# Kernel tuning notes

Measured on AMD Instinct MI355X. Metric: run time of the kernel, lower is better.

Reference implementation:

```python
import jax, jax.numpy as jnp
import numpy as np

B, S, NODE, DEP, R, L, E = 32, 1024, 256, 64, 50, 16, 128


def setup_inputs() -> dict:
    key = jax.random.key(0)
    k1, k2, k3, k4, k5 = jax.random.split(key, 5)
    context = jax.random.normal(k1, (B, S, NODE), dtype=jnp.float32)
    # torch.rand -> uniform [0,1); one [dep, node+dep] matrix per dependency relation
    dep_W = jax.random.uniform(k2, (R, DEP, NODE + DEP), dtype=jnp.float32)
    heads = jax.random.randint(k3, (B, L, E), 0, S, dtype=jnp.int32)
    tails = jax.random.randint(k4, (B, L, E), 0, S, dtype=jnp.int32)
    rels = jax.random.randint(k5, (B, L, E), 0, R, dtype=jnp.int32)
    return {"context": context, "dep_W": dep_W, "heads": heads, "tails": tails, "rels": rels}


def reference(context, dep_W, heads, tails, rels):
    # context: [B,S,node]; dep_W: [R,dep,node+dep]; heads/tails/rels: [B,L,E]
    B_, S_, node = context.shape
    dep = dep_W.shape[1]
    E_ = heads.shape[2]
    batch_off = jnp.arange(B_, dtype=jnp.int32)[:, None] * S_  # [B,1]

    def layer_step(child, layer):
        h, t, r = layer  # each [B,E]
        # gather per-edge tail features (node feature ++ child state from deeper layers)
        ctx_t = jnp.take_along_axis(context, t[:, :, None], axis=1)  # [B,E,node]
        chd_t = jnp.take_along_axis(child, t[:, :, None], axis=1)    # [B,E,dep]
        feat = jnp.concatenate([ctx_t, chd_t], axis=-1)              # [B,E,node+dep]
        W_e = dep_W[r]                                               # [B,E,dep,node+dep]
        # sum(W * feat, dim=1) == relation-indexed matvec
        msg = jnp.einsum('bekd,bed->bek', W_e, feat)                 # [B,E,dep]
        # scatter-average messages onto head nodes (per batch -> flat index)
        idx = (batch_off + h).reshape(-1)                            # [B*E]
        seg = jax.ops.segment_sum(msg.reshape(-1, dep), idx, num_segments=B_ * S_)
        cnt = jax.ops.segment_sum(jnp.ones((B_ * E_,), msg.dtype), idx, num_segments=B_ * S_)
        avg = seg / jnp.maximum(cnt, 1.0)[:, None]
        child_flat = child.reshape(B_ * S_, dep)
        # heads touched this layer get the averaged message (assignment semantics)
        child_new = jnp.where((cnt > 0)[:, None], avg, child_flat).reshape(B_, S_, dep)
        return child_new, None

    child0 = jnp.zeros((B_, S_, dep), context.dtype)
    layers = (jnp.moveaxis(heads, 1, 0), jnp.moveaxis(tails, 1, 0), jnp.moveaxis(rels, 1, 0))
    child, _ = jax.lax.scan(layer_step, child0, layers)  # layer 0 = deepest layer
    return jnp.concatenate([context, child], axis=-1)    # [B,S,node+dep]
```

## Files before the change

kernel.cpp:

```cpp
#include <hip/hip_runtime.h>

constexpr int B_ = 32;
constexpr int S_ = 1024;
constexpr int NODE_ = 256;
constexpr int DEP_ = 64;
constexpr int R_ = 50;
constexpr int L_ = 16;
constexpr int E_ = 128;
constexpr int FEAT_ = NODE_ + DEP_;
constexpr int NEDGE_ = B_ * E_;
constexpr int BS_ = B_ * S_;
constexpr int CH_ = 16;
constexpr int NCH_ = 320;
constexpr int PREB_ = 512;

constexpr size_t N_CHILD  = (size_t)BS_ * DEP_;
constexpr size_t OFF_A0   = N_CHILD;
constexpr size_t OFF_WT   = N_CHILD * 4;
constexpr size_t N_WT     = (size_t)R_ * FEAT_ * DEP_;
constexpr size_t OFF_SORT = OFF_WT + N_WT;
constexpr size_t N_SORT   = (size_t)L_ * NEDGE_;
constexpr size_t OFF_CHUNK= OFF_SORT + N_SORT;
constexpr size_t N_CHUNK_I= (size_t)L_ * NCH_ * 4;
constexpr size_t OFF_HC   = OFF_CHUNK + N_CHUNK_I;
constexpr size_t N_HC     = (size_t)L_ * BS_;
constexpr size_t OFF_MT   = OFF_HC + N_HC;
constexpr size_t OFF_MH   = OFF_MT + N_SORT;
constexpr size_t OFF_MI   = OFF_MH + N_SORT;
constexpr size_t OFF_CD   = OFF_MI + N_SORT;
constexpr size_t N_CD     = (size_t)L_ * NEDGE_ * DEP_;

__global__ void k_pre(const float* __restrict__ W, const int* __restrict__ rels,
                      const int* __restrict__ heads,
                      float* __restrict__ WT2, int* __restrict__ sorted,
                      int4* __restrict__ chunks, int* __restrict__ hc,
                      float* __restrict__ zero_base) {
  int blk = blockIdx.x, tid = threadIdx.x;
  if (blk < L_) {
    int l = blk;
    __shared__ int hist[R_], startA[R_], rank[R_], cstart[R_];
    __shared__ int ntot;
    if (tid < R_) { hist[tid] = 0; rank[tid] = 0; }
    int* hcl = hc + (size_t)l * BS_;
    for (int i = tid; i < BS_; i += 256) hcl[i] = 0;
    __syncthreads();
    for (int ed = tid; ed < NEDGE_; ed += 256) {
      int b = ed >> 7, e = ed & (E_ - 1);
      atomicAdd(&hist[rels[(b * L_ + l) * E_ + e]], 1);
      atomicAdd(&hcl[b * S_ + heads[(b * L_ + l) * E_ + e]], 1);
    }
    __syncthreads();
    if (tid == 0) {
      int s = 0, cs = 0;
      for (int r = 0; r < R_; ++r) {
        startA[r] = s; s += hist[r];
        cstart[r] = cs; cs += (hist[r] + CH_ - 1) / CH_;
      }
      ntot = cs;
    }
    __syncthreads();
    for (int ed = tid; ed < NEDGE_; ed += 256) {
      int b = ed >> 7, e = ed & (E_ - 1);
      int r = rels[(b * L_ + l) * E_ + e];
      int pos = startA[r] + atomicAdd(&rank[r], 1);
      sorted[l * NEDGE_ + pos] = ed;
    }
    if (tid < R_) {
      int n = hist[tid], st = startA[tid], cs = cstart[tid];
      for (int m = 0; m * CH_ < n; ++m) {
        int c = n - m * CH_; if (c > CH_) c = CH_;
        chunks[l * NCH_ + cs + m] = make_int4(tid, st + m * CH_, c, 0);
      }
    }
    __syncthreads();
    for (int i = ntot + tid; i < NCH_; i += 256)
      chunks[l * NCH_ + i] = make_int4(0, 0, 0, 0);
  } else {
    int gtid = (blk - L_) * 256 + tid;
    const int NT = PREB_ * 256;
    for (int gid = gtid; gid < (int)N_WT; gid += NT) {
      int r = gid / 20480;
      int rem = gid - r * 20480;
      int i4 = rem >> 8;
      int k = (rem >> 2) & 63;
      int c = rem & 3;
      WT2[gid] = W[((size_t)r * DEP_ + k) * FEAT_ + 4 * i4 + c];
    }
    float4* z4 = (float4*)zero_base;
    int nz4 = (int)((N_CHILD * 2) / 4);
    for (int i = gtid; i < nz4; i += NT) z4[i] = make_float4(0.f, 0.f, 0.f, 0.f);
  }
}

__device__ __forceinline__ float dot64(const float4* __restrict__ f4,
                                       const float4* __restrict__ w) {
  float a0 = 0.f, a1 = 0.f, a2 = 0.f, a3 = 0.f;
#pragma unroll
  for (int i = 0; i < 16; ++i) {
    float4 f = f4[i];
    a0 = fmaf(w[i].x, f.x, a0);
    a1 = fmaf(w[i].y, f.y, a1);
    a2 = fmaf(w[i].z, f.z, a2);
    a3 = fmaf(w[i].w, f.w, a3);
  }
  return (a0 + a1) + (a2 + a3);
}

__global__ void __launch_bounds__(256) k_ctx(
    const float* __restrict__ context, const float* __restrict__ WT2,
    const int* __restrict__ heads, const int* __restrict__ tails,
    const int* __restrict__ sorted, const int4* __restrict__ chunks,
    const int* __restrict__ hc, float* __restrict__ ctxdot,
    int* __restrict__ m_trow, int* __restrict__ m_hrow,
    float* __restrict__ m_invc) {
  int cid = blockIdx.x;
  int l = cid / NCH_;
  int4 ck = chunks[cid];
  int r = ck.x, start = ck.y, ccnt = ck.z;
  if (ccnt == 0) return;
  int tid = threadIdx.x, s = tid >> 6, k = tid & 63;

  __shared__ float feat[CH_][NODE_];
  __shared__ float part[4][CH_][DEP_];
  __shared__ int trows[CH_];
  __shared__ float invs[CH_];

  if (tid < ccnt) {
    int pos = l * NEDGE_ + start + tid;
    int ed = sorted[pos];
    int b = ed >> 7, e = ed & (E_ - 1);
    int t = tails[(b * L_ + l) * E_ + e];
    int h = heads[(b * L_ + l) * E_ + e];
    int trow = b * S_ + t, hrow = b * S_ + h;
    int tch = (l > 0) && (hc[(size_t)(l - 1) * BS_ + trow] > 0);
    float invc = 1.0f / (float)hc[(size_t)l * BS_ + hrow];
    m_trow[pos] = trow | (tch ? (int)0x80000000 : 0);
    m_hrow[pos] = hrow;
    m_invc[pos] = invc;
    trows[tid] = trow;
    invs[tid] = invc;
  }
  __syncthreads();

  int tr[CH_];
#pragma unroll
  for (int j = 0; j < CH_; ++j) tr[j] = trows[(j < ccnt) ? j : (ccnt - 1)];

  const float4* Wp = (const float4*)WT2 + ((size_t)r * 80 + s * 16) * 64 + k;
  float4 w[16];
#pragma unroll
  for (int i = 0; i < 16; ++i) w[i] = Wp[(size_t)i * 64];

#pragma unroll
  for (int j = 0; j < CH_; ++j)
    feat[j][tid] = context[(size_t)tr[j] * NODE_ + tid];
  __syncthreads();

  for (int j = 0; j < ccnt; ++j)
    part[s][j][k] = dot64((const float4*)&feat[j][s * 64], w);
  __syncthreads();

  for (int idx = tid; idx < ccnt * DEP_; idx += 256) {
    int j = idx >> 6, k2 = idx & 63;
    ctxdot[(size_t)(l * NEDGE_ + start + j) * DEP_ + k2] =
        (part[0][j][k2] + part[1][j][k2] + part[2][j][k2] + part[3][j][k2]) *
        invs[j];
  }
}

__global__ void __launch_bounds__(256) k_layer(
    const float* __restrict__ WT2, float* __restrict__ child,
    const int4* __restrict__ chunks, const int* __restrict__ m_trow,
    const int* __restrict__ m_hrow, const float* __restrict__ m_invc,
    const float* __restrict__ ctxdot, int l,
    const float* __restrict__ Aprev, float* __restrict__ Acur,
    float* __restrict__ Anext) {
  int tid = threadIdx.x;
  int4 ck = chunks[l * NCH_ + blockIdx.x];
  int r = ck.x, start = ck.y, ccnt = ck.z;
  __shared__ float feat[CH_][DEP_];

  if (ccnt > 0) {
    int wv = tid >> 6, k = tid & 63;

    const float4* Wp = (const float4*)WT2 + ((size_t)r * 80 + 64) * 64 + k;
    float4 w[16];
#pragma unroll
    for (int i = 0; i < 16; ++i) w[i] = Wp[(size_t)i * 64];

    int jj[4], valid[4], tch[4], trow[4], hrow[4];
    float invc[4];
#pragma unroll
    for (int u = 0; u < 4; ++u) {
      int j = wv + 4 * u;
      valid[u] = (j < ccnt);
      jj[u] = valid[u] ? j : (ccnt - 1);
      int pos = l * NEDGE_ + start + jj[u];
      int tr = m_trow[pos];
      tch[u] = (tr < 0);
      trow[u] = tr & 0x7fffffff;
      hrow[u] = m_hrow[pos];
      invc[u] = m_invc[pos];
    }

    float v[4];
#pragma unroll
    for (int u = 0; u < 4; ++u) {
      const float* p = tch[u] ? Aprev : child;
      v[u] = p[(size_t)trow[u] * DEP_ + k];
    }
#pragma unroll
    for (int u = 0; u < 4; ++u) feat[jj[u]][k] = v[u];
    __syncthreads();

#pragma unroll
    for (int u = 0; u < 4; ++u) {
      float d = dot64((const float4*)&feat[jj[u]][0], w);
      int pos = l * NEDGE_ + start + jj[u];
      float contrib = d * invc[u] + ctxdot[(size_t)pos * DEP_ + k];
      if (valid[u]) atomicAdd(&Acur[(size_t)hrow[u] * DEP_ + k], contrib);
    }
  }

  int gtid = blockIdx.x * 256 + tid;
  const int NT = NCH_ * 256;
  if (l > 0) {
    const float4* Ap4 = (const float4*)Aprev;
    float4* ch4 = (float4*)child;
    const int* mh = m_hrow + (size_t)(l - 1) * NEDGE_;
    for (int idx = gtid; idx < NEDGE_ * 16; idx += NT) {
      int pos = idx >> 4, c4 = idx & 15;
      int hrow = mh[pos];
      ch4[(size_t)hrow * 16 + c4] = Ap4[(size_t)hrow * 16 + c4];
    }
  }
  if (l + 1 < L_) {
    float4* An4 = (float4*)Anext;
    const int* mh = m_hrow + (size_t)(l + 1) * NEDGE_;
    float4 z = make_float4(0.f, 0.f, 0.f, 0.f);
    for (int idx = gtid; idx < NEDGE_ * 16; idx += NT) {
      int pos = idx >> 4, c4 = idx & 15;
      An4[(size_t)mh[pos] * 16 + c4] = z;
    }
  }
}

__global__ void k_out(const float4* __restrict__ ctx4,
                      const float4* __restrict__ chd4,
                      const float4* __restrict__ A04,
                      const int* __restrict__ hc15,
                      float4* __restrict__ out4) {
  constexpr int TOT4 = B_ * S_ * (FEAT_ / 4);
  int i = blockIdx.x * blockDim.x + threadIdx.x;
  if (i >= TOT4) return;
  int row = i / 80;
  int c4 = i - row * 80;
  float4 v;
  if (c4 < 64) {
    v = ctx4[(size_t)row * 64 + c4];
  } else {
    int k4 = c4 - 64;
    v = (hc15[row] > 0) ? A04[(size_t)row * 16 + k4]
                        : chd4[(size_t)row * 16 + k4];
  }
  out4[i] = v;
}

extern "C" void kernel_launch(void* const* d_in, const int* in_sizes, int n_in,
                              void* d_out, int out_size, void* d_ws, size_t ws_size,
                              hipStream_t stream) {
  const float* context = (const float*)d_in[0];
  const float* dep_W   = (const float*)d_in[1];
  const int*   heads   = (const int*)d_in[2];
  const int*   tails   = (const int*)d_in[3];
  const int*   rels    = (const int*)d_in[4];
  float* out = (float*)d_out;

  float* ws = (float*)d_ws;
  float* child  = ws;
  float* A[3] = { ws + OFF_A0, ws + OFF_A0 + N_CHILD, ws + OFF_A0 + 2 * N_CHILD };
  float* WT2    = ws + OFF_WT;
  int*   sorted = (int*)(ws + OFF_SORT);
  int4*  chunks = (int4*)(ws + OFF_CHUNK);
  int*   hc     = (int*)(ws + OFF_HC);
  int*   m_trow = (int*)(ws + OFF_MT);
  int*   m_hrow = (int*)(ws + OFF_MH);
  float* m_invc = ws + OFF_MI;
  float* ctxdot = ws + OFF_CD;

  k_pre<<<L_ + PREB_, 256, 0, stream>>>(dep_W, rels, heads, WT2, sorted,
                                        chunks, hc, child);

  k_ctx<<<L_ * NCH_, 256, 0, stream>>>(context, WT2, heads, tails, sorted,
                                       chunks, hc, ctxdot, m_trow, m_hrow,
                                       m_invc);

  for (int l = 0; l < L_; ++l) {
    float* Acur  = A[l % 3];
    float* Aprev = A[(l + 2) % 3];
    float* Anext = A[(l + 1) % 3];
    k_layer<<<NCH_, 256, 0, stream>>>(WT2, child, chunks, m_trow, m_hrow,
                                      m_invc, ctxdot, l, Aprev, Acur, Anext);
  }

  constexpr int TOT4 = B_ * S_ * (FEAT_ / 4);
  k_out<<<(TOT4 + 255) / 256, 256, 0, stream>>>(
      (const float4*)context, (const float4*)child, (const float4*)A[0],
      hc + (size_t)(L_ - 1) * BS_, (float4*)out);
}
```

Measured before the change: 313.0 us.

## Fuse per-layer launches and output copy into one cooperative persistent kernel

Replaces the sixteen per-layer kernel launches and the separate output kernel with one cooperative kernel. It loops over layers and uses a grid-wide sync between them, then writes the output at the end. k_ctx and the layer dot products now read context/child rows straight from global memory with wave-uniform indices instead of staging them through shared memory. This removes launch gaps and shared-memory round trips. The cost is that only 256 blocks handle the 320 chunks, and the final copy runs on a smaller grid.

Result: slower. 938.0 us (+199.7%).

```diff
diff --git a/kernel.cpp b/kernel.cpp
--- a/kernel.cpp
+++ b/kernel.cpp
@@ -1,4 +1,7 @@
 #include <hip/hip_runtime.h>
+#include <hip/hip_cooperative_groups.h>
+
+namespace cg = cooperative_groups;
 
 constexpr int B_ = 32;
 constexpr int S_ = 1024;
@@ -13,6 +16,7 @@
 constexpr int CH_ = 16;
 constexpr int NCH_ = 320;
 constexpr int PREB_ = 512;
+constexpr int GRID_ = 256;
 
 constexpr size_t N_CHILD  = (size_t)BS_ * DEP_;
 constexpr size_t OFF_A0   = N_CHILD;
@@ -92,20 +96,6 @@
   }
 }
 
-__device__ __forceinline__ float dot64(const float4* __restrict__ f4,
-                                       const float4* __restrict__ w) {
-  float a0 = 0.f, a1 = 0.f, a2 = 0.f, a3 = 0.f;
-#pragma unroll
-  for (int i = 0; i < 16; ++i) {
-    float4 f = f4[i];
-    a0 = fmaf(w[i].x, f.x, a0);
-    a1 = fmaf(w[i].y, f.y, a1);
-    a2 = fmaf(w[i].z, f.z, a2);
-    a3 = fmaf(w[i].w, f.w, a3);
-  }
-  return (a0 + a1) + (a2 + a3);
-}
-
 __global__ void __launch_bounds__(256) k_ctx(
     const float* __restrict__ context, const float* __restrict__ WT2,
     const int* __restrict__ heads, const int* __restrict__ tails,
@@ -120,9 +110,7 @@
   if (ccnt == 0) return;
   int tid = threadIdx.x, s = tid >> 6, k = tid & 63;
 
-  __shared__ float feat[CH_][NODE_];
   __shared__ float part[4][CH_][DEP_];
-  __shared__ int trows[CH_];
   __shared__ float invs[CH_];
 
   if (tid < ccnt) {
@@ -137,27 +125,34 @@
     m_trow[pos] = trow | (tch ? (int)0x80000000 : 0);
     m_hrow[pos] = hrow;
     m_invc[pos] = invc;
-    trows[tid] = trow;
     invs[tid] = invc;
   }
-  __syncthreads();
-
-  int tr[CH_];
-#pragma unroll
-  for (int j = 0; j < CH_; ++j) tr[j] = trows[(j < ccnt) ? j : (ccnt - 1)];
 
   const float4* Wp = (const float4*)WT2 + ((size_t)r * 80 + s * 16) * 64 + k;
   float4 w[16];
 #pragma unroll
   for (int i = 0; i < 16; ++i) w[i] = Wp[(size_t)i * 64];
 
-#pragma unroll
-  for (int j = 0; j < CH_; ++j)
-    feat[j][tid] = context[(size_t)tr[j] * NODE_ + tid];
-  __syncthreads();
-
-  for (int j = 0; j < ccnt; ++j)
-    part[s][j][k] = dot64((const float4*)&feat[j][s * 64], w);
+#pragma unroll 4
+  for (int j = 0; j < CH_; ++j) {
+    int jc = (j < ccnt) ? j : (ccnt - 1);
+    int pos = l * NEDGE_ + start + jc;
+    int ed = __builtin_amdgcn_readfirstlane(sorted[pos]);
+    int b = ed >> 7, e = ed & (E_ - 1);
+    int t = __builtin_amdgcn_readfirstlane(tails[(b * L_ + l) * E_ + e]);
+    const float4* fp =
+        (const float4*)(context + ((size_t)(b * S_ + t)) * NODE_ + s * 64);
+    float a0 = 0.f, a1 = 0.f, a2 = 0.f, a3 = 0.f;
+#pragma unroll
+    for (int i = 0; i < 16; ++i) {
+      float4 f = fp[i];
+      a0 = fmaf(w[i].x, f.x, a0);
+      a1 = fmaf(w[i].y, f.y, a1);
+      a2 = fmaf(w[i].z, f.z, a2);
+      a3 = fmaf(w[i].w, f.w, a3);
+    }
+    part[s][jc][k] = (a0 + a1) + (a2 + a3);
+  }
   __syncthreads();
 
   for (int idx = tid; idx < ccnt * DEP_; idx += 256) {
@@ -168,102 +163,98 @@
   }
 }
 
-__global__ void __launch_bounds__(256) k_layer(
+__global__ void __launch_bounds__(256) k_chain(
     const float* __restrict__ WT2, float* __restrict__ child,
     const int4* __restrict__ chunks, const int* __restrict__ m_trow,
     const int* __restrict__ m_hrow, const float* __restrict__ m_invc,
-    const float* __restrict__ ctxdot, int l,
-    const float* __restrict__ Aprev, float* __restrict__ Acur,
-    float* __restrict__ Anext) {
-  int tid = threadIdx.x;
-  int4 ck = chunks[l * NCH_ + blockIdx.x];
-  int r = ck.x, start = ck.y, ccnt = ck.z;
-  __shared__ float feat[CH_][DEP_];
-
-  if (ccnt > 0) {
-    int wv = tid >> 6, k = tid & 63;
-
-    const float4* Wp = (const float4*)WT2 + ((size_t)r * 80 + 64) * 64 + k;
-    float4 w[16];
-#pragma unroll
-    for (int i = 0; i < 16; ++i) w[i] = Wp[(size_t)i * 64];
-
-    int jj[4], valid[4], tch[4], trow[4], hrow[4];
-    float invc[4];
-#pragma unroll
-    for (int u = 0; u < 4; ++u) {
-      int j = wv + 4 * u;
-      valid[u] = (j < ccnt);
-      jj[u] = valid[u] ? j : (ccnt - 1);
-      int pos = l * NEDGE_ + start + jj[u];
-      int tr = m_trow[pos];
-      tch[u] = (tr < 0);
-      trow[u] = tr & 0x7fffffff;
-      hrow[u] = m_hrow[pos];
-      invc[u] = m_invc[pos];
-    }
-
-    float v[4];
-#pragma unroll
-    for (int u = 0; u < 4; ++u) {
-      const float* p = tch[u] ? Aprev : child;
-      v[u] = p[(size_t)trow[u] * DEP_ + k];
-    }
-#pragma unroll
-    for (int u = 0; u < 4; ++u) feat[jj[u]][k] = v[u];
-    __syncthreads();
-
-#pragma unroll
-    for (int u = 0; u < 4; ++u) {
-      float d = dot64((const float4*)&feat[jj[u]][0], w);
-      int pos = l * NEDGE_ + start + jj[u];
-      float contrib = d * invc[u] + ctxdot[(size_t)pos * DEP_ + k];
-      if (valid[u]) atomicAdd(&Acur[(size_t)hrow[u] * DEP_ + k], contrib);
-    }
-  }
-
-  int gtid = blockIdx.x * 256 + tid;
-  const int NT = NCH_ * 256;
-  if (l > 0) {
-    const float4* Ap4 = (const float4*)Aprev;
-    float4* ch4 = (float4*)child;
-    const int* mh = m_hrow + (size_t)(l - 1) * NEDGE_;
-    for (int idx = gtid; idx < NEDGE_ * 16; idx += NT) {
-      int pos = idx >> 4, c4 = idx & 15;
-      int hrow = mh[pos];
-      ch4[(size_t)hrow * 16 + c4] = Ap4[(size_t)hrow * 16 + c4];
-    }
-  }
-  if (l + 1 < L_) {
-    float4* An4 = (float4*)Anext;
-    const int* mh = m_hrow + (size_t)(l + 1) * NEDGE_;
-    float4 z = make_float4(0.f, 0.f, 0.f, 0.f);
-    for (int idx = gtid; idx < NEDGE_ * 16; idx += NT) {
-      int pos = idx >> 4, c4 = idx & 15;
-      An4[(size_t)mh[pos] * 16 + c4] = z;
-    }
-  }
-}
-
-__global__ void k_out(const float4* __restrict__ ctx4,
-                      const float4* __restrict__ chd4,
-                      const float4* __restrict__ A04,
-                      const int* __restrict__ hc15,
-                      float4* __restrict__ out4) {
+    const float* __restrict__ ctxdot, float* __restrict__ Abase,
+    const int* __restrict__ hc15, const float4* __restrict__ ctx4,
+    float4* __restrict__ out4) {
+  cg::grid_group grid = cg::this_grid();
+  int tid = threadIdx.x, wv = tid >> 6, k = tid & 63;
+
+  for (int l = 0; l < L_; ++l) {
+    float* Acur        = Abase + (size_t)(l % 3) * N_CHILD;
+    const float* Aprev = Abase + (size_t)((l + 2) % 3) * N_CHILD;
+    float* Anext       = Abase + (size_t)((l + 1) % 3) * N_CHILD;
+
+    for (int cid = blockIdx.x; cid < NCH_; cid += gridDim.x) {
+      int4 ck = chunks[l * NCH_ + cid];
+      int r = ck.x, start = ck.y, ccnt = ck.z;
+      if (ccnt == 0) continue;
+
+      const float4* Wp = (const float4*)WT2 + ((size_t)r * 80 + 64) * 64 + k;
+      float4 w[16];
+#pragma unroll
+      for (int i = 0; i < 16; ++i) w[i] = Wp[(size_t)i * 64];
+
+#pragma unroll
+      for (int u = 0; u < 4; ++u) {
+        int j = wv + 4 * u;
+        bool valid = (j < ccnt);
+        int jc = valid ? j : 0;
+        int pos = l * NEDGE_ + start + jc;
+        int tr = __builtin_amdgcn_readfirstlane(m_trow[pos]);
+        int hrow = __builtin_amdgcn_readfirstlane(m_hrow[pos]);
+        float invc = m_invc[pos];
+        int trow = tr & 0x7fffffff;
+        const float* base = (tr < 0) ? Aprev : child;
+        const float4* fp = (const float4*)(base + (size_t)trow * DEP_);
+        float a0 = 0.f, a1 = 0.f, a2 = 0.f, a3 = 0.f;
+#pragma unroll
+        for (int i = 0; i < 16; ++i) {
+          float4 f = fp[i];
+          a0 = fmaf(w[i].x, f.x, a0);
+          a1 = fmaf(w[i].y, f.y, a1);
+          a2 = fmaf(w[i].z, f.z, a2);
+          a3 = fmaf(w[i].w, f.w, a3);
+        }
+        float d = (a0 + a1) + (a2 + a3);
+        float contrib = d * invc + ctxdot[(size_t)pos * DEP_ + k];
+        if (valid) atomicAdd(&Acur[(size_t)hrow * DEP_ + k], contrib);
+      }
+    }
+
+    int gtid = blockIdx.x * 256 + tid;
+    const int NT = GRID_ * 256;
+    if (l > 0) {
+      const float4* Ap4 = (const float4*)Aprev;
+      float4* ch4 = (float4*)child;
+      const int* mh = m_hrow + (size_t)(l - 1) * NEDGE_;
+      for (int idx = gtid; idx < NEDGE_ * 16; idx += NT) {
+        int pos = idx >> 4, c4 = idx & 15;
+        int hrow = mh[pos];
+        ch4[(size_t)hrow * 16 + c4] = Ap4[(size_t)hrow * 16 + c4];
+      }
+    }
+    if (l + 1 < L_) {
+      float4* An4 = (float4*)Anext;
+      const int* mh = m_hrow + (size_t)(l + 1) * NEDGE_;
+      float4 z = make_float4(0.f, 0.f, 0.f, 0.f);
+      for (int idx = gtid; idx < NEDGE_ * 16; idx += NT) {
+        int pos = idx >> 4, c4 = idx & 15;
+        An4[(size_t)mh[pos] * 16 + c4] = z;
+      }
+    }
+    grid.sync();
+  }
+
   constexpr int TOT4 = B_ * S_ * (FEAT_ / 4);
-  int i = blockIdx.x * blockDim.x + threadIdx.x;
-  if (i >= TOT4) return;
-  int row = i / 80;
-  int c4 = i - row * 80;
-  float4 v;
-  if (c4 < 64) {
-    v = ctx4[(size_t)row * 64 + c4];
-  } else {
-    int k4 = c4 - 64;
-    v = (hc15[row] > 0) ? A04[(size_t)row * 16 + k4]
-                        : chd4[(size_t)row * 16 + k4];
-  }
-  out4[i] = v;
+  const float4* A04 = (const float4*)Abase;
+  const float4* chd4 = (const float4*)child;
+  for (int i = blockIdx.x * 256 + tid; i < TOT4; i += GRID_ * 256) {
+    int row = i / 80;
+    int c4 = i - row * 80;
+    float4 v;
+    if (c4 < 64) {
+      v = ctx4[(size_t)row * 64 + c4];
+    } else {
+      int k4 = c4 - 64;
+      v = (hc15[row] > 0) ? A04[(size_t)row * 16 + k4]
+                          : chd4[(size_t)row * 16 + k4];
+    }
+    out4[i] = v;
+  }
 }
 
 extern "C" void kernel_launch(void* const* d_in, const int* in_sizes, int n_in,
@@ -278,7 +269,7 @@
 
   float* ws = (float*)d_ws;
   float* child  = ws;
-  float* A[3] = { ws + OFF_A0, ws + OFF_A0 + N_CHILD, ws + OFF_A0 + 2 * N_CHILD };
+  float* Abase  = ws + OFF_A0;
   float* WT2    = ws + OFF_WT;
   int*   sorted = (int*)(ws + OFF_SORT);
   int4*  chunks = (int4*)(ws + OFF_CHUNK);
@@ -295,16 +286,18 @@
                                        chunks, hc, ctxdot, m_trow, m_hrow,
                                        m_invc);
 
-  for (int l = 0; l < L_; ++l) {
-    float* Acur  = A[l % 3];
-    float* Aprev = A[(l + 2) % 3];
-    float* Anext = A[(l + 1) % 3];
-    k_layer<<<NCH_, 256, 0, stream>>>(WT2, child, chunks, m_trow, m_hrow,
-                                      m_invc, ctxdot, l, Aprev, Acur, Anext);
-  }
-
-  constexpr int TOT4 = B_ * S_ * (FEAT_ / 4);
-  k_out<<<(TOT4 + 255) / 256, 256, 0, stream>>>(
-      (const float4*)context, (const float4*)child, (const float4*)A[0],
-      hc + (size_t)(L_ - 1) * BS_, (float4*)out);
+  {
+    const int4* chunks_c = chunks;
+    const int* mt = m_trow; const int* mh = m_hrow;
+    const float* mi = m_invc; const float* cd = ctxdot;
+    const float* wt = WT2;
+    const int* hc15 = hc + (size_t)(L_ - 1) * BS_;
+    const float4* ctx4 = (const float4*)context;
+    float4* out4 = (float4*)out;
+    void* args[] = { (void*)&wt, (void*)&child, (void*)&chunks_c, (void*)&mt,
+                     (void*)&mh, (void*)&mi, (void*)&cd, (void*)&Abase,
+                     (void*)&hc15, (void*)&ctx4, (void*)&out4 };
+    hipLaunchCooperativeKernel((const void*)k_chain, dim3(GRID_), dim3(256),
+                               args, 0, stream);
+  }
 }
```
